# Kernel tuning notes

Measured on AMD Instinct MI355X. Metric: run time of the kernel, lower is better.

Reference implementation:

```python
import jax, jax.numpy as jnp
import numpy as np

DIM = 1024
NUM_HEAD = 16
DIM_HEAD = DIM // NUM_HEAD
RMS_EPS = 1.1920929e-07  # torch.finfo(float32).eps (nn.RMSNorm default eps=None)
EPS_LIN = 1e-6
THETA = 10000.0


def rmsnorm(x, g, eps=RMS_EPS):
    return x * jax.lax.rsqrt(jnp.mean(x * x, axis=-1, keepdims=True) + eps) * g


def rope_cos_sin(seq_len, dim_head, dtype=jnp.float32):
    inv_freq = 1.0 / (THETA ** (jnp.arange(0, dim_head, 2, dtype=dtype) / dim_head))
    t = jnp.arange(seq_len, dtype=dtype)
    freqs = jnp.outer(t, inv_freq)  # [L, dh//2]
    return jnp.cos(freqs), jnp.sin(freqs)


def apply_rope(t, cos, sin):
    # t: [b, h, L, dh]; pairs are (t[...,2i], t[...,2i+1]) viewed as complex
    tr = t[..., 0::2]
    ti = t[..., 1::2]
    out_r = tr * cos - ti * sin
    out_i = tr * sin + ti * cos
    return jnp.stack([out_r, out_i], axis=-1).reshape(t.shape)


def setup_inputs() -> dict:
    key = jax.random.key(0)
    ks = jax.random.split(key, 5)
    B, L = 4, 4096
    x = jax.random.normal(ks[0], (B, L, DIM), dtype=jnp.float32)
    Wqkv = jax.random.normal(ks[1], (3 * DIM, DIM), dtype=jnp.float32) * 0.02
    bqkv = jax.random.normal(ks[2], (3 * DIM,), dtype=jnp.float32) * 0.02
    gq = jnp.ones((DIM,), dtype=jnp.float32)
    gk = jnp.ones((DIM,), dtype=jnp.float32)
    Wout = jax.random.normal(ks[3], (DIM, DIM), dtype=jnp.float32) * 0.02
    bout = jax.random.normal(ks[4], (DIM,), dtype=jnp.float32) * 0.02
    gout = jnp.ones((DIM,), dtype=jnp.float32)
    return {"x": x, "Wqkv": Wqkv, "bqkv": bqkv, "gq": gq, "gk": gk,
            "Wout": Wout, "bout": bout, "gout": gout}


def reference(x, Wqkv, bqkv, gq, gk, Wout, bout, gout):
    B, L, D = x.shape
    qkv = x @ Wqkv.T + bqkv  # [B, L, 3D]
    q, k, v = jnp.split(qkv, 3, axis=-1)
    q = rmsnorm(q, gq)
    k = rmsnorm(k, gk)
    # b L (h d) -> b h L d
    split = lambda t: t.reshape(B, L, NUM_HEAD, DIM_HEAD).transpose(0, 2, 1, 3)
    q, k, v = split(q), split(k), split(v)
    cos, sin = rope_cos_sin(L, DIM_HEAD)  # start_pos = 0 (default)
    cos = cos[None, None]  # [1,1,L,dh//2]
    sin = sin[None, None]
    q = apply_rope(q, cos, sin)
    k = apply_rope(k, cos, sin)
    # linear attention: ReLU feature map + padded-value normalization trick
    qf = jax.nn.relu(q)
    kf = jax.nn.relu(k)
    vpad = jnp.concatenate([v, jnp.ones_like(v[..., :1])], axis=-1)  # pad_val=1.0
    vk = jnp.einsum('bhlp,bhld->bhpd', vpad, kf)       # [b,h,dh+1,dh]
    res = jnp.einsum('bhpd,bhld->bhlp', vk, qf)        # [b,h,L,dh+1]
    attn = res[..., :-1] / (res[..., -1:] + EPS_LIN)
    attn = attn.transpose(0, 2, 1, 3).reshape(B, L, D)  # b h L d -> b L (h d)
    out = rmsnorm(attn @ Wout.T + bout, gout)
    return out
```

## Files before the change

### kernel.cpp

```cpp
#include <hip/hip_runtime.h>
#include <stdint.h>

#define RMS_EPS 1.1920929e-07f
#define EPS_LIN 1e-6f

typedef __attribute__((ext_vector_type(8))) short bf16x8;
typedef __attribute__((ext_vector_type(4))) float f32x4;

__device__ __forceinline__ unsigned short f2bf(float f) {
  union { float f; unsigned int u; } v; v.f = f;
  unsigned int r = v.u + 0x7fffu + ((v.u >> 16) & 1u);
  return (unsigned short)(r >> 16);
}
__device__ __forceinline__ float bf2f(unsigned short s) {
  union { unsigned int u; float f; } v; v.u = ((unsigned int)s) << 16;
  return v.f;
}

__global__ __launch_bounds__(256) void k_init(
    const float* __restrict__ x, const float* __restrict__ Wqkv,
    const float* __restrict__ Wout,
    unsigned short* __restrict__ xb, unsigned short* __restrict__ wqkvb,
    unsigned short* __restrict__ woutb,
    float* __restrict__ cosT, float* __restrict__ sinT,
    float* __restrict__ vkbuf) {
  const int blk = blockIdx.x;
  const int t = threadIdx.x;
  if (blk < 20480) {
    const float* src;
    unsigned short* dst;
    int base;
    if (blk < 16384) { src = x; dst = xb; base = blk; }
    else if (blk < 19456) { src = Wqkv; dst = wqkvb; base = blk - 16384; }
    else { src = Wout; dst = woutb; base = blk - 19456; }
    int i = (base * 256 + t) * 4;
    float4 v = *reinterpret_cast<const float4*>(src + i);
    ushort4 o = { f2bf(v.x), f2bf(v.y), f2bf(v.z), f2bf(v.w) };
    *reinterpret_cast<ushort4*>(dst + i) = o;
  } else if (blk < 20992) {
    int idx = (blk - 20480) * 256 + t;
    int l = idx >> 5, i = idx & 31;
    float inv_freq = expf(-((float)(2 * i) / 64.0f) * logf(10000.0f));
    float ang = (float)l * inv_freq;
    cosT[idx] = cosf(ang);
    sinT[idx] = sinf(ang);
  } else {
    int i = ((blk - 20992) * 256 + t) * 4;
    if (i < 64 * 65 * 64) {
      float4 z = { 0.f, 0.f, 0.f, 0.f };
      *reinterpret_cast<float4*>(vkbuf + i) = z;
    }
  }
}

__device__ __forceinline__ void stage16(const unsigned short* g, unsigned short* lds_base,
                                        int lane) {
#if __has_builtin(__builtin_amdgcn_global_load_lds)
  __builtin_amdgcn_global_load_lds(
      (const __attribute__((address_space(1))) unsigned int*)g,
      (__attribute__((address_space(3))) unsigned int*)lds_base, 16, 0, 0);
#else
  *reinterpret_cast<uint4*>(lds_base + lane * 8) = *reinterpret_cast<const uint4*>(g);
#endif
}

__global__ __launch_bounds__(256, 3) void k_gemm_bt(
    const unsigned short* __restrict__ A, const unsigned short* __restrict__ Bw,
    const float* __restrict__ bias, int M, int N, int K, int mode,
    unsigned short* __restrict__ qb, unsigned short* __restrict__ kb,
    unsigned short* __restrict__ vb, unsigned short* __restrict__ preb) {
  __shared__ unsigned short As[128 * 64];
  __shared__ unsigned short Bs[128 * 64];
  const int nt = N >> 7;
  const int bm = blockIdx.x / nt, bn = blockIdx.x % nt;
  const int m0 = bm << 7, n0 = bn << 7;
  const int t = threadIdx.x;
  const int wave = t >> 6, lane = t & 63;
  const int wr = wave >> 1, wc = wave & 1;
  const int quad = lane >> 4, m16 = lane & 15;

  const unsigned short* ApS[4];
  const unsigned short* BpS[4];
  unsigned short* AlS[4];
  unsigned short* BlS[4];
#pragma unroll
  for (int s = 0; s < 4; ++s) {
    int u = wave * 256 + s * 64 + lane;
    int row = u >> 3;
    int ku = (u & 7) ^ (row & 7);
    ApS[s] = A + (size_t)(m0 + row) * K + ku * 8;
    BpS[s] = Bw + (size_t)(n0 + row) * K + ku * 8;
    AlS[s] = As + (size_t)(wave * 256 + s * 64) * 8;
    BlS[s] = Bs + (size_t)(wave * 256 + s * 64) * 8;
  }

  int offA[4][2], offB[4][2];
#pragma unroll
  for (int i = 0; i < 4; ++i) {
    int rowA = wr * 64 + i * 16 + m16;
    int rowB = wc * 64 + i * 16 + m16;
#pragma unroll
    for (int ks = 0; ks < 2; ++ks) {
      int kuf = ks * 4 + quad;
      offA[i][ks] = (rowA * 8 + (kuf ^ (rowA & 7))) * 8;
      offB[i][ks] = (rowB * 8 + (kuf ^ (rowB & 7))) * 8;
    }
  }

  f32x4 acc[4][4] = {};

  for (int k0 = 0; k0 < K; k0 += 64) {
#pragma unroll
    for (int s = 0; s < 4; ++s) {
      stage16(ApS[s] + k0, AlS[s], lane);
      stage16(BpS[s] + k0, BlS[s], lane);
    }
    __syncthreads();
#pragma unroll
    for (int ks = 0; ks < 2; ++ks) {
      bf16x8 fa[4], fb[4];
#pragma unroll
      for (int i = 0; i < 4; ++i)
        fa[i] = *reinterpret_cast<const bf16x8*>(As + offA[i][ks]);
#pragma unroll
      for (int j = 0; j < 4; ++j)
        fb[j] = *reinterpret_cast<const bf16x8*>(Bs + offB[j][ks]);
#pragma unroll
      for (int i = 0; i < 4; ++i)
#pragma unroll
        for (int j = 0; j < 4; ++j)
          acc[i][j] = __builtin_amdgcn_mfma_f32_16x16x32_bf16(fa[i], fb[j], acc[i][j], 0, 0, 0);
    }
    __syncthreads();
  }

#pragma unroll
  for (int i = 0; i < 4; ++i) {
    int rbase = m0 + wr * 64 + i * 16 + quad * 4;
#pragma unroll
    for (int j = 0; j < 4; ++j) {
      int col = n0 + wc * 64 + j * 16 + m16;
      float bc = bias[col];
#pragma unroll
      for (int r = 0; r < 4; ++r) {
        int row = rbase + r;
        float val = acc[i][j][r] + bc;
        unsigned short bv = f2bf(val);
        if (mode == 0) {
          if (col < 1024) {
            qb[(size_t)row * 1024 + col] = bv;
          } else if (col < 2048) {
            kb[(size_t)row * 1024 + (col - 1024)] = bv;
          } else {
            int h = (col - 2048) >> 6, d = col & 63;
            int b = row >> 12, l = row & 4095;
            vb[(((size_t)(b * 16 + h)) * 4096 + l) * 64 + d] = bv;
          }
        } else {
          preb[(size_t)row * N + col] = bv;
        }
      }
    }
  }
}

__global__ __launch_bounds__(256) void k_qknorm(
    const unsigned short* __restrict__ qb, const unsigned short* __restrict__ kb,
    const float* __restrict__ gq, const float* __restrict__ gk,
    const float* __restrict__ cosT, const float* __restrict__ sinT,
    unsigned short* __restrict__ qfb, unsigned short* __restrict__ kfb) {
  const int wid = (blockIdx.x << 2) + (threadIdx.x >> 6);
  const int row = wid >> 1;
  const int which = wid & 1;
  const int lane = threadIdx.x & 63;
  const int l = row & 4095;
  const int b = row >> 12;
  const unsigned short* src = (which ? kb : qb) + (size_t)row * 1024;
  const float* g = which ? gk : gq;
  unsigned short* dstb = which ? kfb : qfb;

  float v[16];
  float ss = 0.f;
#pragma unroll
  for (int c = 0; c < 4; ++c) {
    int d = c * 256 + lane * 4;
    ushort4 u = *reinterpret_cast<const ushort4*>(src + d);
    float a0 = bf2f(u.x), a1 = bf2f(u.y), a2 = bf2f(u.z), a3 = bf2f(u.w);
    v[c * 4 + 0] = a0; v[c * 4 + 1] = a1; v[c * 4 + 2] = a2; v[c * 4 + 3] = a3;
    ss += a0 * a0 + a1 * a1 + a2 * a2 + a3 * a3;
  }
#pragma unroll
  for (int off = 1; off < 64; off <<= 1) ss += __shfl_xor(ss, off, 64);
  const float sc = rsqrtf(ss * (1.0f / 1024.0f) + RMS_EPS);

#pragma unroll
  for (int c = 0; c < 4; ++c) {
    int d = c * 256 + lane * 4;
    int i0 = (d & 63) >> 1;
    float c0 = cosT[l * 32 + i0], s0 = sinT[l * 32 + i0];
    float c1 = cosT[l * 32 + i0 + 1], s1 = sinT[l * 32 + i0 + 1];
    float x0 = v[c * 4 + 0] * sc * g[d];
    float x1 = v[c * 4 + 1] * sc * g[d + 1];
    float x2 = v[c * 4 + 2] * sc * g[d + 2];
    float x3 = v[c * 4 + 3] * sc * g[d + 3];
    float r0 = x0 * c0 - x1 * s0, r1 = x0 * s0 + x1 * c0;
    float r2 = x2 * c1 - x3 * s1, r3 = x2 * s1 + x3 * c1;
    ushort4 o = { f2bf(fmaxf(r0, 0.f)), f2bf(fmaxf(r1, 0.f)),
                  f2bf(fmaxf(r2, 0.f)), f2bf(fmaxf(r3, 0.f)) };
    int h = d >> 6;
    *reinterpret_cast<ushort4*>(dstb + (((size_t)(b * 16 + h)) * 4096 + l) * 64 + (d & 63)) = o;
  }
}

__global__ __launch_bounds__(256) void k_vk(const unsigned short* __restrict__ vb,
                                            const unsigned short* __restrict__ kfb,
                                            float* __restrict__ part) {
  const int bh = blockIdx.x >> 4;
  const int chunk = blockIdx.x & 15;
  const int t = threadIdx.x;
  const int wv = t >> 6, lane = t & 63;
  const int quad = lane >> 4, m16 = lane & 15;

  __shared__ __align__(16) unsigned short Vt[64 * 40];
  __shared__ __align__(16) unsigned short Kt[64 * 40];
  __shared__ float dred[4][64];

  f32x4 acc[4] = {};
  float accD = 0.f;

  for (int tile = 0; tile < 8; ++tile) {
    const size_t rbase =
        ((size_t)bh * 4096 + chunk * 256 + tile * 32 + wv * 8) * 64 + lane;
    bf16x8 vv, kv;
#pragma unroll
    for (int j = 0; j < 8; ++j) {
      unsigned short ve = vb[rbase + j * 64];
      unsigned short ke = kfb[rbase + j * 64];
      vv[j] = (short)ve;
      kv[j] = (short)ke;
      accD += bf2f(ke);
    }
    *reinterpret_cast<bf16x8*>(Vt + lane * 40 + wv * 8) = vv;
    *reinterpret_cast<bf16x8*>(Kt + lane * 40 + wv * 8) = kv;
    __syncthreads();

    bf16x8 fa = *reinterpret_cast<const bf16x8*>(Vt + (wv * 16 + m16) * 40 + quad * 8);
#pragma unroll
    for (int j = 0; j < 4; ++j) {
      bf16x8 fb = *reinterpret_cast<const bf16x8*>(Kt + (j * 16 + m16) * 40 + quad * 8);
      acc[j] = __builtin_amdgcn_mfma_f32_16x16x32_bf16(fa, fb, acc[j], 0, 0, 0);
    }
    __syncthreads();
  }

  float* dst = part + ((size_t)chunk * 64 + bh) * 4160;
#pragma unroll
  for (int j = 0; j < 4; ++j)
#pragma unroll
    for (int r = 0; r < 4; ++r)
      dst[(wv * 16 + quad * 4 + r) * 64 + j * 16 + m16] = acc[j][r];

  dred[wv][lane] = accD;
  __syncthreads();
  if (t < 64) dst[64 * 64 + t] = dred[0][t] + dred[1][t] + dred[2][t] + dred[3][t];
}

__global__ __launch_bounds__(256) void k_vkred(const float* __restrict__ part,
                                               float* __restrict__ vk) {
  const int i = (blockIdx.x * 256 + threadIdx.x) * 4;
  float4 s = *reinterpret_cast<const float4*>(part + i);
#pragma unroll
  for (int c = 1; c < 16; ++c) {
    float4 r = *reinterpret_cast<const float4*>(part + (size_t)c * 266240 + i);
    s.x += r.x; s.y += r.y; s.z += r.z; s.w += r.w;
  }
  *reinterpret_cast<float4*>(vk + i) = s;
}

__global__ __launch_bounds__(256) void k_res(const unsigned short* __restrict__ qfb,
                                             const float* __restrict__ vk,
                                             unsigned short* __restrict__ attnb) {
  const int bh = blockIdx.x >> 5;
  const int lt = (blockIdx.x & 31) << 7;
  const int b = bh >> 4, h = bh & 15;
  const int t = threadIdx.x;
  const int wave = t >> 6, lane = t & 63;
  __shared__ unsigned short Aq[128 * 64];
  __shared__ unsigned short Bv[64 * 64];
  __shared__ float vkD[64];
  __shared__ float invden[128];

  const unsigned short* Ag = qfb + ((size_t)bh * 4096 + lt) * 64;
#pragma unroll
  for (int s = 0; s < 4; ++s)
    stage16(Ag + wave * 2048 + s * 512 + lane * 8, Aq + wave * 2048 + s * 512, lane);

  const float* vsrc = vk + (size_t)bh * 65 * 64;
  {
    int base = t * 16;
#pragma unroll
    for (int c = 0; c < 4; ++c) {
      float4 f = *reinterpret_cast<const float4*>(vsrc + base + c * 4);
      ushort4 o = { f2bf(f.x), f2bf(f.y), f2bf(f.z), f2bf(f.w) };
      *reinterpret_cast<ushort4*>(Bv + base + c * 4) = o;
    }
  }
  if (t < 64) vkD[t] = vsrc[64 * 64 + t];
  __syncthreads();

  f32x4 acc[2][4] = {};
  const int quad = lane >> 4, m16 = lane & 15;
#pragma unroll
  for (int step = 0; step < 2; ++step) {
    bf16x8 fa[2], fb[4];
#pragma unroll
    for (int i = 0; i < 2; ++i)
      fa[i] = *reinterpret_cast<const bf16x8*>(Aq + (wave * 32 + i * 16 + m16) * 64 +
                                               step * 32 + quad * 8);
#pragma unroll
    for (int j = 0; j < 4; ++j)
      fb[j] = *reinterpret_cast<const bf16x8*>(Bv + (j * 16 + m16) * 64 +
                                               step * 32 + quad * 8);
#pragma unroll
    for (int i = 0; i < 2; ++i)
#pragma unroll
      for (int j = 0; j < 4; ++j)
        acc[i][j] = __builtin_amdgcn_mfma_f32_16x16x32_bf16(fa[i], fb[j], acc[i][j], 0, 0, 0);
  }

  {
    const unsigned short* qr = Aq + (t >> 1) * 64 + (t & 1) * 32;
    const float* vd = vkD + (t & 1) * 32;
    float ds = 0.f;
#pragma unroll
    for (int c = 0; c < 4; ++c) {
      bf16x8 qv = *reinterpret_cast<const bf16x8*>(qr + c * 8);
#pragma unroll
      for (int j = 0; j < 8; ++j)
        ds += bf2f((unsigned short)qv[j]) * vd[c * 8 + j];
    }
    ds += __shfl_xor(ds, 1, 64);
    if ((t & 1) == 0) invden[t >> 1] = 1.0f / (ds + EPS_LIN);
  }
  __syncthreads();

#pragma unroll
  for (int i = 0; i < 2; ++i) {
#pragma unroll
    for (int r = 0; r < 4; ++r) {
      int row = wave * 32 + i * 16 + quad * 4 + r;
      float inv = invden[row];
      unsigned short* dst = attnb + ((size_t)(b * 4096 + lt + row)) * 1024 + h * 64;
#pragma unroll
      for (int j = 0; j < 4; ++j)
        dst[j * 16 + m16] = f2bf(acc[i][j][r] * inv);
    }
  }
}

__global__ __launch_bounds__(256) void k_outnorm(const unsigned short* __restrict__ preb,
                                                 const float* __restrict__ gout,
                                                 float* __restrict__ out) {
  const int row = (blockIdx.x << 2) + (threadIdx.x >> 6);
  const int lane = threadIdx.x & 63;
  const unsigned short* src = preb + (size_t)row * 1024;
  float* drow = out + (size_t)row * 1024;
  float v[16];
  float ss = 0.f;
#pragma unroll
  for (int c = 0; c < 4; ++c) {
    int d = c * 256 + lane * 4;
    ushort4 u = *reinterpret_cast<const ushort4*>(src + d);
    float a0 = bf2f(u.x), a1 = bf2f(u.y), a2 = bf2f(u.z), a3 = bf2f(u.w);
    v[c * 4 + 0] = a0; v[c * 4 + 1] = a1; v[c * 4 + 2] = a2; v[c * 4 + 3] = a3;
    ss += a0 * a0 + a1 * a1 + a2 * a2 + a3 * a3;
  }
#pragma unroll
  for (int off = 1; off < 64; off <<= 1) ss += __shfl_xor(ss, off, 64);
  const float sc = rsqrtf(ss * (1.0f / 1024.0f) + RMS_EPS);
#pragma unroll
  for (int c = 0; c < 4; ++c) {
    int d = c * 256 + lane * 4;
    float4 o = { v[c * 4 + 0] * sc * gout[d], v[c * 4 + 1] * sc * gout[d + 1],
                 v[c * 4 + 2] * sc * gout[d + 2], v[c * 4 + 3] * sc * gout[d + 3] };
    *reinterpret_cast<float4*>(drow + d) = o;
  }
}

#define OFF_XB     0ull
#define OFF_WQKVB  33554432ull
#define OFF_WOUTB  39845888ull
#define OFF_QB     41943040ull
#define OFF_KB     75497472ull
#define OFF_VB     109051904ull
#define OFF_QFB    142606336ull
#define OFF_KFB    176160768ull
#define OFF_VK     209715200ull
#define OFF_ATTNB  210780160ull
#define OFF_COST   244334592ull
#define OFF_SINT   244858880ull
#define WS_NEEDED  245383168ull

extern "C" void kernel_launch(void* const* d_in, const int* in_sizes, int n_in,
                              void* d_out, int out_size, void* d_ws, size_t ws_size,
                              hipStream_t stream) {
  const float* x    = (const float*)d_in[0];
  const float* Wqkv = (const float*)d_in[1];
  const float* bqkv = (const float*)d_in[2];
  const float* gq   = (const float*)d_in[3];
  const float* gk   = (const float*)d_in[4];
  const float* Wout = (const float*)d_in[5];
  const float* bout = (const float*)d_in[6];
  const float* gout = (const float*)d_in[7];

  if (ws_size < WS_NEEDED) return;

  char* ws = (char*)d_ws;
  unsigned short* xb    = (unsigned short*)(ws + OFF_XB);
  unsigned short* wqkvb = (unsigned short*)(ws + OFF_WQKVB);
  unsigned short* woutb = (unsigned short*)(ws + OFF_WOUTB);
  unsigned short* qb    = (unsigned short*)(ws + OFF_QB);
  unsigned short* kb    = (unsigned short*)(ws + OFF_KB);
  unsigned short* vb    = (unsigned short*)(ws + OFF_VB);
  unsigned short* qfb   = (unsigned short*)(ws + OFF_QFB);
  unsigned short* kfb   = (unsigned short*)(ws + OFF_KFB);
  float*          vkbuf = (float*)(ws + OFF_VK);
  unsigned short* attnb = (unsigned short*)(ws + OFF_ATTNB);
  float*          cosT  = (float*)(ws + OFF_COST);
  float*          sinT  = (float*)(ws + OFF_SINT);
  unsigned short* preb  = (unsigned short*)(ws + OFF_QB);
  float*          vkpart = (float*)(ws + OFF_ATTNB);

  k_init<<<21252, 256, 0, stream>>>(x, Wqkv, Wout, xb, wqkvb, woutb, cosT, sinT, vkbuf);

  k_gemm_bt<<<128 * 24, 256, 0, stream>>>(xb, wqkvb, bqkv, 16384, 3072, 1024, 0,
                                          qb, kb, vb, nullptr);
  k_qknorm<<<8192, 256, 0, stream>>>(qb, kb, gq, gk, cosT, sinT, qfb, kfb);

  k_vk<<<1024, 256, 0, stream>>>(vb, kfb, vkpart);
  k_vkred<<<260, 256, 0, stream>>>(vkpart, vkbuf);

  k_res<<<2048, 256, 0, stream>>>(qfb, vkbuf, attnb);

  k_gemm_bt<<<128 * 8, 256, 0, stream>>>(attnb, woutb, bout, 16384, 1024, 1024, 1,
                                         nullptr, nullptr, nullptr, preb);
  k_outnorm<<<4096, 256, 0, stream>>>(preb, gout, (float*)d_out);
}
```

Before: 370.4 us.

## Split-K output GEMM, remap workgroups across XCDs, vectorize norm kernels

The output projection GEMM is split into two K-halves, giving 2048 workgroups instead of 1024. Each half writes its own bf16 partial buffer, and k_outnorm sums the two partials before the RMS norm, with the bias added only by the first half. Both GEMMs remap block indices so that consecutive tiles are spread across the eight XCD groups. k_qknorm and k_outnorm now use 16-byte vector loads and stores with a contiguous per-lane layout, and the zeroing of vkbuf in k_init is dropped. The bf16 rounding of each partial adds some precision loss, and removing the zeroing assumes the reduction kernel fully overwrites vkbuf.

```diff
diff --git a/kernel.cpp b/kernel.cpp
--- a/kernel.cpp
+++ b/kernel.cpp
@@ -22,8 +22,7 @@
     const float* __restrict__ Wout,
     unsigned short* __restrict__ xb, unsigned short* __restrict__ wqkvb,
     unsigned short* __restrict__ woutb,
-    float* __restrict__ cosT, float* __restrict__ sinT,
-    float* __restrict__ vkbuf) {
+    float* __restrict__ cosT, float* __restrict__ sinT) {
   const int blk = blockIdx.x;
   const int t = threadIdx.x;
   if (blk < 20480) {
@@ -37,19 +36,13 @@
     float4 v = *reinterpret_cast<const float4*>(src + i);
     ushort4 o = { f2bf(v.x), f2bf(v.y), f2bf(v.z), f2bf(v.w) };
     *reinterpret_cast<ushort4*>(dst + i) = o;
-  } else if (blk < 20992) {
+  } else {
     int idx = (blk - 20480) * 256 + t;
     int l = idx >> 5, i = idx & 31;
     float inv_freq = expf(-((float)(2 * i) / 64.0f) * logf(10000.0f));
     float ang = (float)l * inv_freq;
     cosT[idx] = cosf(ang);
     sinT[idx] = sinf(ang);
-  } else {
-    int i = ((blk - 20992) * 256 + t) * 4;
-    if (i < 64 * 65 * 64) {
-      float4 z = { 0.f, 0.f, 0.f, 0.f };
-      *reinterpret_cast<float4*>(vkbuf + i) = z;
-    }
   }
 }
 
@@ -72,8 +65,14 @@
   __shared__ unsigned short As[128 * 64];
   __shared__ unsigned short Bs[128 * 64];
   const int nt = N >> 7;
-  const int bm = blockIdx.x / nt, bn = blockIdx.x % nt;
+  const int nwg = gridDim.x;
+  const int wg = (blockIdx.x & 7) * (nwg >> 3) + (blockIdx.x >> 3);
+  int ksplit = 0, tile = wg;
+  if (mode == 1) { ksplit = wg >> 10; tile = wg & 1023; }
+  const int bm = tile / nt, bn = tile % nt;
   const int m0 = bm << 7, n0 = bn << 7;
+  const int kbeg = (mode == 1) ? (ksplit << 9) : 0;
+  const int kend = (mode == 1) ? (kbeg + 512) : K;
   const int t = threadIdx.x;
   const int wave = t >> 6, lane = t & 63;
   const int wr = wave >> 1, wc = wave & 1;
@@ -109,7 +108,7 @@
 
   f32x4 acc[4][4] = {};
 
-  for (int k0 = 0; k0 < K; k0 += 64) {
+  for (int k0 = kbeg; k0 < kend; k0 += 64) {
 #pragma unroll
     for (int s = 0; s < 4; ++s) {
       stage16(ApS[s] + k0, AlS[s], lane);
@@ -134,13 +133,14 @@
     __syncthreads();
   }
 
+  unsigned short* po = preb + (size_t)ksplit * 16777216ull;
 #pragma unroll
   for (int i = 0; i < 4; ++i) {
     int rbase = m0 + wr * 64 + i * 16 + quad * 4;
 #pragma unroll
     for (int j = 0; j < 4; ++j) {
       int col = n0 + wc * 64 + j * 16 + m16;
-      float bc = bias[col];
+      float bc = (mode == 0 || ksplit == 0) ? bias[col] : 0.f;
 #pragma unroll
       for (int r = 0; r < 4; ++r) {
         int row = rbase + r;
@@ -157,7 +157,7 @@
             vb[(((size_t)(b * 16 + h)) * 4096 + l) * 64 + d] = bv;
           }
         } else {
-          preb[(size_t)row * N + col] = bv;
+          po[(size_t)row * N + col] = bv;
         }
       }
     }
@@ -175,41 +175,45 @@
   const int lane = threadIdx.x & 63;
   const int l = row & 4095;
   const int b = row >> 12;
-  const unsigned short* src = (which ? kb : qb) + (size_t)row * 1024;
+  const unsigned short* src = (which ? kb : qb) + (size_t)row * 1024 + lane * 16;
   const float* g = which ? gk : gq;
   unsigned short* dstb = which ? kfb : qfb;
 
+  bf16x8 u0 = *reinterpret_cast<const bf16x8*>(src);
+  bf16x8 u1 = *reinterpret_cast<const bf16x8*>(src + 8);
   float v[16];
   float ss = 0.f;
 #pragma unroll
-  for (int c = 0; c < 4; ++c) {
-    int d = c * 256 + lane * 4;
-    ushort4 u = *reinterpret_cast<const ushort4*>(src + d);
-    float a0 = bf2f(u.x), a1 = bf2f(u.y), a2 = bf2f(u.z), a3 = bf2f(u.w);
-    v[c * 4 + 0] = a0; v[c * 4 + 1] = a1; v[c * 4 + 2] = a2; v[c * 4 + 3] = a3;
-    ss += a0 * a0 + a1 * a1 + a2 * a2 + a3 * a3;
-  }
+  for (int e = 0; e < 8; ++e) {
+    v[e] = bf2f((unsigned short)u0[e]);
+    v[8 + e] = bf2f((unsigned short)u1[e]);
+  }
+#pragma unroll
+  for (int e = 0; e < 16; ++e) ss += v[e] * v[e];
 #pragma unroll
   for (int off = 1; off < 64; off <<= 1) ss += __shfl_xor(ss, off, 64);
   const float sc = rsqrtf(ss * (1.0f / 1024.0f) + RMS_EPS);
 
-#pragma unroll
-  for (int c = 0; c < 4; ++c) {
-    int d = c * 256 + lane * 4;
-    int i0 = (d & 63) >> 1;
-    float c0 = cosT[l * 32 + i0], s0 = sinT[l * 32 + i0];
-    float c1 = cosT[l * 32 + i0 + 1], s1 = sinT[l * 32 + i0 + 1];
-    float x0 = v[c * 4 + 0] * sc * g[d];
-    float x1 = v[c * 4 + 1] * sc * g[d + 1];
-    float x2 = v[c * 4 + 2] * sc * g[d + 2];
-    float x3 = v[c * 4 + 3] * sc * g[d + 3];
-    float r0 = x0 * c0 - x1 * s0, r1 = x0 * s0 + x1 * c0;
-    float r2 = x2 * c1 - x3 * s1, r3 = x2 * s1 + x3 * c1;
-    ushort4 o = { f2bf(fmaxf(r0, 0.f)), f2bf(fmaxf(r1, 0.f)),
-                  f2bf(fmaxf(r2, 0.f)), f2bf(fmaxf(r3, 0.f)) };
-    int h = d >> 6;
-    *reinterpret_cast<ushort4*>(dstb + (((size_t)(b * 16 + h)) * 4096 + l) * 64 + (d & 63)) = o;
-  }
+  const float* gp = g + lane * 16;
+  const float* cp = cosT + l * 32 + (lane & 3) * 8;
+  const float* sp = sinT + l * 32 + (lane & 3) * 8;
+  bf16x8 o0, o1;
+#pragma unroll
+  for (int p = 0; p < 8; ++p) {
+    float cc = cp[p], sv = sp[p];
+    float x0 = v[2 * p] * sc * gp[2 * p];
+    float x1 = v[2 * p + 1] * sc * gp[2 * p + 1];
+    float r0 = x0 * cc - x1 * sv;
+    float r1 = x0 * sv + x1 * cc;
+    unsigned short b0 = f2bf(fmaxf(r0, 0.f));
+    unsigned short b1 = f2bf(fmaxf(r1, 0.f));
+    if (p < 4) { o0[2 * p] = (short)b0; o0[2 * p + 1] = (short)b1; }
+    else { o1[2 * (p - 4)] = (short)b0; o1[2 * (p - 4) + 1] = (short)b1; }
+  }
+  unsigned short* dp =
+      dstb + (((size_t)(b * 16 + (lane >> 2))) * 4096 + l) * 64 + (lane & 3) * 16;
+  *reinterpret_cast<bf16x8*>(dp) = o0;
+  *reinterpret_cast<bf16x8*>(dp + 8) = o1;
 }
 
 __global__ __launch_bounds__(256) void k_vk(const unsigned short* __restrict__ vb,
@@ -358,32 +362,37 @@
   }
 }
 
-__global__ __launch_bounds__(256) void k_outnorm(const unsigned short* __restrict__ preb,
+__global__ __launch_bounds__(256) void k_outnorm(const unsigned short* __restrict__ preb0,
+                                                 const unsigned short* __restrict__ preb1,
                                                  const float* __restrict__ gout,
                                                  float* __restrict__ out) {
   const int row = (blockIdx.x << 2) + (threadIdx.x >> 6);
   const int lane = threadIdx.x & 63;
-  const unsigned short* src = preb + (size_t)row * 1024;
-  float* drow = out + (size_t)row * 1024;
+  const unsigned short* s0 = preb0 + (size_t)row * 1024 + lane * 16;
+  const unsigned short* s1 = preb1 + (size_t)row * 1024 + lane * 16;
+  float* drow = out + (size_t)row * 1024 + lane * 16;
+  bf16x8 a0 = *reinterpret_cast<const bf16x8*>(s0);
+  bf16x8 a1 = *reinterpret_cast<const bf16x8*>(s0 + 8);
+  bf16x8 b0 = *reinterpret_cast<const bf16x8*>(s1);
+  bf16x8 b1 = *reinterpret_cast<const bf16x8*>(s1 + 8);
   float v[16];
   float ss = 0.f;
 #pragma unroll
-  for (int c = 0; c < 4; ++c) {
-    int d = c * 256 + lane * 4;
-    ushort4 u = *reinterpret_cast<const ushort4*>(src + d);
-    float a0 = bf2f(u.x), a1 = bf2f(u.y), a2 = bf2f(u.z), a3 = bf2f(u.w);
-    v[c * 4 + 0] = a0; v[c * 4 + 1] = a1; v[c * 4 + 2] = a2; v[c * 4 + 3] = a3;
-    ss += a0 * a0 + a1 * a1 + a2 * a2 + a3 * a3;
-  }
+  for (int e = 0; e < 8; ++e) {
+    v[e] = bf2f((unsigned short)a0[e]) + bf2f((unsigned short)b0[e]);
+    v[8 + e] = bf2f((unsigned short)a1[e]) + bf2f((unsigned short)b1[e]);
+  }
+#pragma unroll
+  for (int e = 0; e < 16; ++e) ss += v[e] * v[e];
 #pragma unroll
   for (int off = 1; off < 64; off <<= 1) ss += __shfl_xor(ss, off, 64);
   const float sc = rsqrtf(ss * (1.0f / 1024.0f) + RMS_EPS);
+  const float* gp = gout + lane * 16;
 #pragma unroll
   for (int c = 0; c < 4; ++c) {
-    int d = c * 256 + lane * 4;
-    float4 o = { v[c * 4 + 0] * sc * gout[d], v[c * 4 + 1] * sc * gout[d + 1],
-                 v[c * 4 + 2] * sc * gout[d + 2], v[c * 4 + 3] * sc * gout[d + 3] };
-    *reinterpret_cast<float4*>(drow + d) = o;
+    float4 o = { v[c * 4 + 0] * sc * gp[c * 4 + 0], v[c * 4 + 1] * sc * gp[c * 4 + 1],
+                 v[c * 4 + 2] * sc * gp[c * 4 + 2], v[c * 4 + 3] * sc * gp[c * 4 + 3] };
+    *reinterpret_cast<float4*>(drow + c * 4) = o;
   }
 }
 
@@ -428,10 +437,11 @@
   unsigned short* attnb = (unsigned short*)(ws + OFF_ATTNB);
   float*          cosT  = (float*)(ws + OFF_COST);
   float*          sinT  = (float*)(ws + OFF_SINT);
-  unsigned short* preb  = (unsigned short*)(ws + OFF_QB);
+  unsigned short* preb0 = (unsigned short*)(ws + OFF_QB);
+  unsigned short* preb1 = (unsigned short*)(ws + OFF_KB);
   float*          vkpart = (float*)(ws + OFF_ATTNB);
 
-  k_init<<<21252, 256, 0, stream>>>(x, Wqkv, Wout, xb, wqkvb, woutb, cosT, sinT, vkbuf);
+  k_init<<<20992, 256, 0, stream>>>(x, Wqkv, Wout, xb, wqkvb, woutb, cosT, sinT);
 
   k_gemm_bt<<<128 * 24, 256, 0, stream>>>(xb, wqkvb, bqkv, 16384, 3072, 1024, 0,
                                           qb, kb, vb, nullptr);
@@ -442,7 +452,7 @@
 
   k_res<<<2048, 256, 0, stream>>>(qfb, vkbuf, attnb);
 
-  k_gemm_bt<<<128 * 8, 256, 0, stream>>>(attnb, woutb, bout, 16384, 1024, 1024, 1,
-                                         nullptr, nullptr, nullptr, preb);
-  k_outnorm<<<4096, 256, 0, stream>>>(preb, gout, (float*)d_out);
-}
+  k_gemm_bt<<<2048, 256, 0, stream>>>(attnb, woutb, bout, 16384, 1024, 1024, 1,
+                                      nullptr, nullptr, nullptr, preb0);
+  k_outnorm<<<4096, 256, 0, stream>>>(preb0, preb1, gout, (float*)d_out);
+}
```

After: 386.1 us. 1.04x slower.
